# Performance work log

Hardware: AMD Instinct MI355X
Metric: run time of the kernel (lower is better)

The kernel has to match this reference:

```python
import jax, jax.numpy as jnp
import numpy as np

E = 8        # num_experts
C = 1024     # n_emb
H = 4096     # n_emb * ff_mult
B, T = 4, 1024


def setup_inputs() -> dict:
    key = jax.random.key(0)
    k_x, k_g, k_1, k_2, k_3 = jax.random.split(key, 5)
    scale = 0.02
    return {
        "x": jax.random.normal(k_x, (B, T, C), dtype=jnp.float32),
        "Wg": jax.random.normal(k_g, (E, C), dtype=jnp.float32) * scale,   # gate: Linear(C, E), weight [E, C]
        "W1": jax.random.normal(k_1, (E, C, H), dtype=jnp.float32) * scale,  # per-expert w1 (transposed for einsum)
        "W2": jax.random.normal(k_2, (E, H, C), dtype=jnp.float32) * scale,  # per-expert w2
        "W3": jax.random.normal(k_3, (E, C, H), dtype=jnp.float32) * scale,  # per-expert w3
        "top_k": 2,
    }


def reference(x, Wg, W1, W2, W3, top_k):
    Bd, Td, Cd = x.shape
    xf = x.reshape(-1, Cd)                                   # [N, C]
    N = xf.shape[0]
    logits = jnp.einsum('nc,ec->ne', xf, Wg)                 # router logits [N, E]
    probs = jax.nn.softmax(logits.astype(jnp.float32), axis=-1)
    w, sel = jax.lax.top_k(probs, top_k)                     # [N, k]
    w = w / w.sum(axis=-1, keepdims=True)                    # renormalize over selected
    # combine weight per (token, expert): sum of normalized topk weights routed to e
    cw = jnp.zeros((N, E), jnp.float32).at[jnp.arange(N)[:, None], sel].add(w)
    # dense grouped SwiGLU over all experts; combine weights zero out unselected experts
    h1 = jnp.einsum('nc,ech->neh', xf, W1)                   # [N, E, H]
    g = jax.nn.silu(h1) * jnp.einsum('nc,ech->neh', xf, W3)  # [N, E, H]
    out = jnp.einsum('neh,ehc,ne->nc', g, W2, cw.astype(x.dtype))
    return out.reshape(Bd, Td, Cd)
```

## Files before the change

### kernel.cpp

```cpp
#include <hip/hip_runtime.h>
#include <hip/hip_bf16.h>

#define E_     8
#define C_     1024
#define H_     4096
#define N_TOK  4096
#define TOPK   2
#define NSLOT  (N_TOK*TOPK)
#define SPAD   (NSLOT+128)

#define BM 128
#define BN 128
#define BK 32
#define LPAD 40

typedef __attribute__((ext_vector_type(4))) float f32x4;
typedef __attribute__((ext_vector_type(8))) short short8;

__device__ __forceinline__ unsigned short f2bf(float f) {
    return __builtin_bit_cast(unsigned short, __float2bfloat16(f));
}

__device__ __forceinline__ void gload16(const void* g, const void* l) {
    __builtin_amdgcn_global_load_lds(
        (const __attribute__((address_space(1))) unsigned int*)g,
        (__attribute__((address_space(3))) unsigned int*)l, 16, 0, 0);
}

__global__ void router_kernel(const float* __restrict__ x, const float* __restrict__ Wg,
                              int* __restrict__ sel, float* __restrict__ wts) {
    int wave = (blockIdx.x * blockDim.x + threadIdx.x) >> 6;
    int lane = threadIdx.x & 63;
    if (wave >= N_TOK) return;
    const float* xr = x + (size_t)wave * C_;
    float acc[E_];
#pragma unroll
    for (int e = 0; e < E_; ++e) acc[e] = 0.f;
    for (int c = lane; c < C_; c += 64) {
        float xv = xr[c];
#pragma unroll
        for (int e = 0; e < E_; ++e) acc[e] += xv * Wg[e * C_ + c];
    }
#pragma unroll
    for (int e = 0; e < E_; ++e) {
#pragma unroll
        for (int off = 32; off > 0; off >>= 1) acc[e] += __shfl_xor(acc[e], off);
    }
    if (lane == 0) {
        float mx = acc[0];
#pragma unroll
        for (int e = 1; e < E_; ++e) mx = fmaxf(mx, acc[e]);
        float p[E_]; float s = 0.f;
#pragma unroll
        for (int e = 0; e < E_; ++e) { p[e] = __expf(acc[e] - mx); s += p[e]; }
        float inv = 1.f / s;
#pragma unroll
        for (int e = 0; e < E_; ++e) p[e] *= inv;
        int b0 = 0; float v0 = p[0];
#pragma unroll
        for (int e = 1; e < E_; ++e) if (p[e] > v0) { v0 = p[e]; b0 = e; }
        int b1 = -1; float v1 = -1.f;
#pragma unroll
        for (int e = 0; e < E_; ++e) { if (e != b0 && p[e] > v1) { v1 = p[e]; b1 = e; } }
        float isum = 1.f / (v0 + v1);
        sel[wave*2]   = b0; sel[wave*2+1] = b1;
        wts[wave*2]   = v0 * isum; wts[wave*2+1] = v1 * isum;
    }
}

__global__ void assign_kernel(const int* __restrict__ sel, const float* __restrict__ wts,
                              int* __restrict__ counts, int* __restrict__ offsets,
                              int* __restrict__ pos_of_slot, int* __restrict__ token_of,
                              float* __restrict__ slotw) {
    __shared__ int cnt[256][E_];
    __shared__ int offs[E_];
    int t = threadIdx.x;
    const int PER = NSLOT / 256;
    int base = t * PER;
    int loc[E_];
#pragma unroll
    for (int e = 0; e < E_; ++e) loc[e] = 0;
    for (int i = 0; i < PER; ++i) loc[sel[base + i]]++;
#pragma unroll
    for (int e = 0; e < E_; ++e) cnt[t][e] = loc[e];
    __syncthreads();
    if (t < E_) {
        int run = 0;
        for (int i = 0; i < 256; ++i) { int c = cnt[i][t]; cnt[i][t] = run; run += c; }
        counts[t] = run;
    }
    __syncthreads();
    if (t == 0) {
        int s = 0;
        for (int e = 0; e < E_; ++e) { offs[e] = s; offsets[e] = s; s += counts[e]; }
    }
    __syncthreads();
    int run[E_];
#pragma unroll
    for (int e = 0; e < E_; ++e) run[e] = offs[e] + cnt[t][e];
    for (int i = 0; i < PER; ++i) {
        int s = base + i;
        int e = sel[s];
        int p = run[e]++;
        pos_of_slot[s] = p;
        token_of[p] = s >> 1;
        slotw[p] = wts[s];
    }
}

__global__ void copy_kernel(const float* __restrict__ x, const int* __restrict__ pos_of_slot,
                            unsigned short* __restrict__ Xg) {
    int slot = blockIdx.x * 4 + (threadIdx.x >> 6);
    int lane = threadIdx.x & 63;
    int pos = pos_of_slot[slot];
    int n = slot >> 1;
    const float* xr = x + (size_t)n * C_;
    unsigned short* dst = Xg + (size_t)pos * C_;
#pragma unroll
    for (int i = 0; i < 4; ++i) {
        int c0 = i * 256 + lane * 4;
        float4 v = *(const float4*)(xr + c0);
        ushort4 b;
        b.x = f2bf(v.x); b.y = f2bf(v.y); b.z = f2bf(v.z); b.w = f2bf(v.w);
        *(ushort4*)(dst + c0) = b;
    }
}

__global__ void wconv_kernel(const float* __restrict__ src, unsigned short* __restrict__ dst,
                             int R, int Cc) {
    int e = blockIdx.z;
    int c0 = blockIdx.x * 64;
    int r0 = blockIdx.y * 64;
    const float* s = src + (size_t)e * R * Cc;
    unsigned short* d = dst + (size_t)e * R * Cc;
    __shared__ unsigned short t_[64][72];
    int t = threadIdx.x;
    int tr = t >> 4, tc4 = (t & 15) * 4;
#pragma unroll
    for (int i = 0; i < 4; ++i) {
        int r = tr + i * 16;
        float4 v = *(const float4*)(s + (size_t)(r0 + r) * Cc + c0 + tc4);
        t_[r][tc4+0] = f2bf(v.x); t_[r][tc4+1] = f2bf(v.y);
        t_[r][tc4+2] = f2bf(v.z); t_[r][tc4+3] = f2bf(v.w);
    }
    __syncthreads();
    int oc = t >> 2, seg = (t & 3) * 16;
    short8 w0, w1;
#pragma unroll
    for (int j = 0; j < 8; ++j) {
        w0[j] = (short)t_[seg + j][oc];
        w1[j] = (short)t_[seg + 8 + j][oc];
    }
    unsigned short* dp = d + (size_t)(c0 + oc) * R + r0 + seg;
    *(short8*)dp = w0;
    *(short8*)(dp + 8) = w1;
}


__global__ __launch_bounds__(256, 2) void gemm1_fast(
        const unsigned short* __restrict__ Xg, const unsigned short* __restrict__ W1t,
        const unsigned short* __restrict__ W3t, unsigned short* __restrict__ G,
        const int* __restrict__ counts, const int* __restrict__ offsets) {
    int ct = blockIdx.x;
    int rslot = blockIdx.y;
    int e = rslot >> 5, rt = rslot & 31;
    int ne = counts[e];
    if (rt * BM >= ne) return;
    int row0 = offsets[e] + rt * BM;
    int n0 = ct * BN;

    __shared__ unsigned short As[BM * BK];
    __shared__ unsigned short B1s[BN * BK];
    __shared__ unsigned short B3s[BN * BK];

    int tid = threadIdx.x;
    int lane = tid & 63, wid = tid >> 6;
    int wr = (wid >> 1) * 64, wc = (wid & 1) * 64;

    f32x4 acc1[4][4], acc3[4][4];
#pragma unroll
    for (int m = 0; m < 4; ++m)
#pragma unroll
        for (int n = 0; n < 4; ++n) {
            acc1[m][n] = (f32x4){0.f,0.f,0.f,0.f};
            acc3[m][n] = (f32x4){0.f,0.f,0.f,0.f};
        }

    const unsigned short* B1p = W1t + ((size_t)e * H_ + n0) * C_;
    const unsigned short* B3p = W3t + ((size_t)e * H_ + n0) * C_;

    int q = lane >> 4, fr = lane & 15;

    for (int k0 = 0; k0 < C_; k0 += BK) {
#pragma unroll
        for (int h = 0; h < 2; ++h) {
            int cid = h * 4 + wid;
            int row = cid * 16 + (lane >> 2);
            int kc  = (lane & 3) ^ ((row >> 1) & 3);
            gload16(Xg + (size_t)(row0 + row) * C_ + k0 + kc * 8,
                    (const char*)As + cid * 1024);
            gload16(B1p + (size_t)row * C_ + k0 + kc * 8,
                    (const char*)B1s + cid * 1024);
            gload16(B3p + (size_t)row * C_ + k0 + kc * 8,
                    (const char*)B3s + cid * 1024);
        }
        __syncthreads();
        short8 a[4], b1[4], b3[4];
#pragma unroll
        for (int m = 0; m < 4; ++m) {
            int row = wr + m * 16 + fr;
            a[m] = *(const short8*)((const char*)As + row * 64 + ((q ^ ((row >> 1) & 3)) << 4));
        }
#pragma unroll
        for (int n = 0; n < 4; ++n) {
            int row = wc + n * 16 + fr;
            int sw = (q ^ ((row >> 1) & 3)) << 4;
            b1[n] = *(const short8*)((const char*)B1s + row * 64 + sw);
            b3[n] = *(const short8*)((const char*)B3s + row * 64 + sw);
        }
#pragma unroll
        for (int m = 0; m < 4; ++m)
#pragma unroll
            for (int n = 0; n < 4; ++n) {
                acc1[m][n] = __builtin_amdgcn_mfma_f32_16x16x32_bf16(a[m], b1[n], acc1[m][n], 0, 0, 0);
                acc3[m][n] = __builtin_amdgcn_mfma_f32_16x16x32_bf16(a[m], b3[n], acc3[m][n], 0, 0, 0);
            }
        __syncthreads();
    }
    int cfr = lane & 15;
#pragma unroll
    for (int m = 0; m < 4; ++m) {
#pragma unroll
        for (int rg = 0; rg < 4; ++rg) {
            int row = wr + m * 16 + q * 4 + rg;
            if (rt * BM + row < ne) {
                size_t gbase = (size_t)(row0 + row) * H_ + n0;
#pragma unroll
                for (int n = 0; n < 4; ++n) {
                    float h1 = acc1[m][n][rg];
                    float h3 = acc3[m][n][rg];
                    float g = h1 * h3 / (1.f + __expf(-h1));
                    G[gbase + wc + n * 16 + cfr] = f2bf(g);
                }
            }
        }
    }
}

__global__ __launch_bounds__(256, 2) void gemm2_fast(
        const unsigned short* __restrict__ G, const unsigned short* __restrict__ W2t,
        float* __restrict__ out, const int* __restrict__ counts,
        const int* __restrict__ offsets, const int* __restrict__ token_of,
        const float* __restrict__ slotw) {
    int ct = blockIdx.x;
    int rslot = blockIdx.y;
    int e = rslot >> 5, rt = rslot & 31;
    int ne = counts[e];
    if (rt * BM >= ne) return;
    int row0 = offsets[e] + rt * BM;
    int n0 = ct * BN;

    __shared__ unsigned short As[BM * BK];
    __shared__ unsigned short Bs[BN * BK];

    int tid = threadIdx.x;
    int lane = tid & 63, wid = tid >> 6;
    int wr = (wid >> 1) * 64, wc = (wid & 1) * 64;

    f32x4 acc[4][4];
#pragma unroll
    for (int m = 0; m < 4; ++m)
#pragma unroll
        for (int n = 0; n < 4; ++n) acc[m][n] = (f32x4){0.f,0.f,0.f,0.f};

    const unsigned short* Bp = W2t + ((size_t)e * C_ + n0) * H_;
    int q = lane >> 4, fr = lane & 15;

    for (int k0 = 0; k0 < H_; k0 += BK) {
#pragma unroll
        for (int h = 0; h < 2; ++h) {
            int cid = h * 4 + wid;
            int row = cid * 16 + (lane >> 2);
            int kc  = (lane & 3) ^ ((row >> 1) & 3);
            gload16(G + (size_t)(row0 + row) * H_ + k0 + kc * 8,
                    (const char*)As + cid * 1024);
            gload16(Bp + (size_t)row * H_ + k0 + kc * 8,
                    (const char*)Bs + cid * 1024);
        }
        __syncthreads();
        short8 a[4], b[4];
#pragma unroll
        for (int m = 0; m < 4; ++m) {
            int row = wr + m * 16 + fr;
            a[m] = *(const short8*)((const char*)As + row * 64 + ((q ^ ((row >> 1) & 3)) << 4));
        }
#pragma unroll
        for (int n = 0; n < 4; ++n) {
            int row = wc + n * 16 + fr;
            b[n] = *(const short8*)((const char*)Bs + row * 64 + ((q ^ ((row >> 1) & 3)) << 4));
        }
#pragma unroll
        for (int m = 0; m < 4; ++m)
#pragma unroll
            for (int n = 0; n < 4; ++n)
                acc[m][n] = __builtin_amdgcn_mfma_f32_16x16x32_bf16(a[m], b[n], acc[m][n], 0, 0, 0);
        __syncthreads();
    }
    int cfr = lane & 15;
#pragma unroll
    for (int m = 0; m < 4; ++m) {
#pragma unroll
        for (int rg = 0; rg < 4; ++rg) {
            int row = wr + m * 16 + q * 4 + rg;
            if (rt * BM + row < ne) {
                int grow = row0 + row;
                int tok = token_of[grow];
                float w = slotw[grow];
                float* orow = out + (size_t)tok * C_ + n0;
#pragma unroll
                for (int n = 0; n < 4; ++n)
                    atomicAdd(orow + wc + n * 16 + cfr, acc[m][n][rg] * w);
            }
        }
    }
}

__global__ __launch_bounds__(256, 2) void gemm1_slow(
        const unsigned short* __restrict__ Xg, const float* __restrict__ W1,
        const float* __restrict__ W3, unsigned short* __restrict__ G,
        const int* __restrict__ counts, const int* __restrict__ offsets) {
    int ct = blockIdx.x;
    int rslot = blockIdx.y;
    int e = rslot >> 5, rt = rslot & 31;
    int ne = counts[e];
    if (rt * BM >= ne) return;
    int row0 = offsets[e] + rt * BM;
    int n0 = ct * BN;

    __shared__ unsigned short As[BM][LPAD];
    __shared__ unsigned short B1s[BN][LPAD];
    __shared__ unsigned short B3s[BN][LPAD];

    int tid = threadIdx.x;
    int lane = tid & 63, wid = tid >> 6;
    int wr = (wid >> 1) * 64, wc = (wid & 1) * 64;

    f32x4 acc1[4][4], acc3[4][4];
#pragma unroll
    for (int m = 0; m < 4; ++m)
#pragma unroll
        for (int n = 0; n < 4; ++n) {
            acc1[m][n] = (f32x4){0.f,0.f,0.f,0.f};
            acc3[m][n] = (f32x4){0.f,0.f,0.f,0.f};
        }

    const float* B1p = W1 + (size_t)e * C_ * H_ + n0;
    const float* B3p = W3 + (size_t)e * C_ * H_ + n0;
    int chunk = tid & 3, rr = tid >> 2;
    int kq = tid >> 5, n4 = tid & 31;

    for (int k0 = 0; k0 < C_; k0 += BK) {
        __syncthreads();
#pragma unroll
        for (int h = 0; h < 2; ++h) {
            int row = rr + h * 64;
            uint4 v = *(const uint4*)(Xg + (size_t)(row0 + row) * C_ + k0 + chunk * 8);
            *(uint4*)&As[row][chunk * 8] = v;
        }
        {
            float4 r0 = *(const float4*)(B1p + (size_t)(k0 + kq*4 + 0) * H_ + n4*4);
            float4 r1 = *(const float4*)(B1p + (size_t)(k0 + kq*4 + 1) * H_ + n4*4);
            float4 r2 = *(const float4*)(B1p + (size_t)(k0 + kq*4 + 2) * H_ + n4*4);
            float4 r3 = *(const float4*)(B1p + (size_t)(k0 + kq*4 + 3) * H_ + n4*4);
            ushort4 w0 = {f2bf(r0.x), f2bf(r1.x), f2bf(r2.x), f2bf(r3.x)};
            ushort4 w1 = {f2bf(r0.y), f2bf(r1.y), f2bf(r2.y), f2bf(r3.y)};
            ushort4 w2 = {f2bf(r0.z), f2bf(r1.z), f2bf(r2.z), f2bf(r3.z)};
            ushort4 w3 = {f2bf(r0.w), f2bf(r1.w), f2bf(r2.w), f2bf(r3.w)};
            *(ushort4*)&B1s[n4*4+0][kq*4] = w0;
            *(ushort4*)&B1s[n4*4+1][kq*4] = w1;
            *(ushort4*)&B1s[n4*4+2][kq*4] = w2;
            *(ushort4*)&B1s[n4*4+3][kq*4] = w3;
            r0 = *(const float4*)(B3p + (size_t)(k0 + kq*4 + 0) * H_ + n4*4);
            r1 = *(const float4*)(B3p + (size_t)(k0 + kq*4 + 1) * H_ + n4*4);
            r2 = *(const float4*)(B3p + (size_t)(k0 + kq*4 + 2) * H_ + n4*4);
            r3 = *(const float4*)(B3p + (size_t)(k0 + kq*4 + 3) * H_ + n4*4);
            w0 = (ushort4){f2bf(r0.x), f2bf(r1.x), f2bf(r2.x), f2bf(r3.x)};
            w1 = (ushort4){f2bf(r0.y), f2bf(r1.y), f2bf(r2.y), f2bf(r3.y)};
            w2 = (ushort4){f2bf(r0.z), f2bf(r1.z), f2bf(r2.z), f2bf(r3.z)};
            w3 = (ushort4){f2bf(r0.w), f2bf(r1.w), f2bf(r2.w), f2bf(r3.w)};
            *(ushort4*)&B3s[n4*4+0][kq*4] = w0;
            *(ushort4*)&B3s[n4*4+1][kq*4] = w1;
            *(ushort4*)&B3s[n4*4+2][kq*4] = w2;
            *(ushort4*)&B3s[n4*4+3][kq*4] = w3;
        }
        __syncthreads();
        int q = lane >> 4, fr = lane & 15;
        short8 a[4], b1[4], b3[4];
#pragma unroll
        for (int m = 0; m < 4; ++m) a[m] = *(const short8*)&As[wr + m*16 + fr][q*8];
#pragma unroll
        for (int n = 0; n < 4; ++n) {
            b1[n] = *(const short8*)&B1s[wc + n*16 + fr][q*8];
            b3[n] = *(const short8*)&B3s[wc + n*16 + fr][q*8];
        }
#pragma unroll
        for (int m = 0; m < 4; ++m)
#pragma unroll
            for (int n = 0; n < 4; ++n) {
                acc1[m][n] = __builtin_amdgcn_mfma_f32_16x16x32_bf16(a[m], b1[n], acc1[m][n], 0, 0, 0);
                acc3[m][n] = __builtin_amdgcn_mfma_f32_16x16x32_bf16(a[m], b3[n], acc3[m][n], 0, 0, 0);
            }
    }
    int q = lane >> 4, cfr = lane & 15;
#pragma unroll
    for (int m = 0; m < 4; ++m) {
#pragma unroll
        for (int rg = 0; rg < 4; ++rg) {
            int row = wr + m*16 + q*4 + rg;
            if (rt * BM + row < ne) {
                size_t gbase = (size_t)(row0 + row) * H_ + n0;
#pragma unroll
                for (int n = 0; n < 4; ++n) {
                    float h1 = acc1[m][n][rg];
                    float h3 = acc3[m][n][rg];
                    float g = h1 * h3 / (1.f + __expf(-h1));
                    G[gbase + wc + n*16 + cfr] = f2bf(g);
                }
            }
        }
    }
}

__global__ __launch_bounds__(256, 2) void gemm2_slow(
        const unsigned short* __restrict__ G, const float* __restrict__ W2,
        float* __restrict__ out, const int* __restrict__ counts,
        const int* __restrict__ offsets, const int* __restrict__ token_of,
        const float* __restrict__ slotw) {
    int ct = blockIdx.x;
    int rslot = blockIdx.y;
    int e = rslot >> 5, rt = rslot & 31;
    int ne = counts[e];
    if (rt * BM >= ne) return;
    int row0 = offsets[e] + rt * BM;
    int n0 = ct * BN;

    __shared__ unsigned short As[BM][LPAD];
    __shared__ unsigned short Bs[BN][LPAD];

    int tid = threadIdx.x;
    int lane = tid & 63, wid = tid >> 6;
    int wr = (wid >> 1) * 64, wc = (wid & 1) * 64;

    f32x4 acc[4][4];
#pragma unroll
    for (int m = 0; m < 4; ++m)
#pragma unroll
        for (int n = 0; n < 4; ++n) acc[m][n] = (f32x4){0.f,0.f,0.f,0.f};

    const float* Bp = W2 + (size_t)e * H_ * C_ + n0;
    int chunk = tid & 3, rr = tid >> 2;
    int kq = tid >> 5, n4 = tid & 31;

    for (int k0 = 0; k0 < H_; k0 += BK) {
        __syncthreads();
#pragma unroll
        for (int h = 0; h < 2; ++h) {
            int row = rr + h * 64;
            uint4 v = *(const uint4*)(G + (size_t)(row0 + row) * H_ + k0 + chunk * 8);
            *(uint4*)&As[row][chunk * 8] = v;
        }
        {
            float4 r0 = *(const float4*)(Bp + (size_t)(k0 + kq*4 + 0) * C_ + n4*4);
            float4 r1 = *(const float4*)(Bp + (size_t)(k0 + kq*4 + 1) * C_ + n4*4);
            float4 r2 = *(const float4*)(Bp + (size_t)(k0 + kq*4 + 2) * C_ + n4*4);
            float4 r3 = *(const float4*)(Bp + (size_t)(k0 + kq*4 + 3) * C_ + n4*4);
            ushort4 w0 = {f2bf(r0.x), f2bf(r1.x), f2bf(r2.x), f2bf(r3.x)};
            ushort4 w1 = {f2bf(r0.y), f2bf(r1.y), f2bf(r2.y), f2bf(r3.y)};
            ushort4 w2 = {f2bf(r0.z), f2bf(r1.z), f2bf(r2.z), f2bf(r3.z)};
            ushort4 w3 = {f2bf(r0.w), f2bf(r1.w), f2bf(r2.w), f2bf(r3.w)};
            *(ushort4*)&Bs[n4*4+0][kq*4] = w0;
            *(ushort4*)&Bs[n4*4+1][kq*4] = w1;
            *(ushort4*)&Bs[n4*4+2][kq*4] = w2;
            *(ushort4*)&Bs[n4*4+3][kq*4] = w3;
        }
        __syncthreads();
        int q = lane >> 4, fr = lane & 15;
        short8 a[4], b[4];
#pragma unroll
        for (int m = 0; m < 4; ++m) a[m] = *(const short8*)&As[wr + m*16 + fr][q*8];
#pragma unroll
        for (int n = 0; n < 4; ++n) b[n] = *(const short8*)&Bs[wc + n*16 + fr][q*8];
#pragma unroll
        for (int m = 0; m < 4; ++m)
#pragma unroll
            for (int n = 0; n < 4; ++n)
                acc[m][n] = __builtin_amdgcn_mfma_f32_16x16x32_bf16(a[m], b[n], acc[m][n], 0, 0, 0);
    }
    int q = lane >> 4, cfr = lane & 15;
#pragma unroll
    for (int m = 0; m < 4; ++m) {
#pragma unroll
        for (int rg = 0; rg < 4; ++rg) {
            int row = wr + m*16 + q*4 + rg;
            if (rt * BM + row < ne) {
                int grow = row0 + row;
                int tok = token_of[grow];
                float w = slotw[grow];
                float* orow = out + (size_t)tok * C_ + n0;
#pragma unroll
                for (int n = 0; n < 4; ++n)
                    atomicAdd(orow + wc + n*16 + cfr, acc[m][n][rg] * w);
            }
        }
    }
}

extern "C" void kernel_launch(void* const* d_in, const int* in_sizes, int n_in,
                              void* d_out, int out_size, void* d_ws, size_t ws_size,
                              hipStream_t stream) {
    const float* x  = (const float*)d_in[0];
    const float* Wg = (const float*)d_in[1];
    const float* W1 = (const float*)d_in[2];
    const float* W2 = (const float*)d_in[3];
    const float* W3 = (const float*)d_in[4];
    float* out = (float*)d_out;

    char* ws = (char*)d_ws;
    size_t o = 0;
    int*   sel      = (int*)(ws + o);  o += (size_t)NSLOT * 4;
    float* wts      = (float*)(ws + o); o += (size_t)NSLOT * 4;
    int*   pos      = (int*)(ws + o);  o += (size_t)NSLOT * 4;
    int*   token_of = (int*)(ws + o);  o += (size_t)NSLOT * 4;
    float* slotw    = (float*)(ws + o); o += (size_t)NSLOT * 4;
    int*   counts   = (int*)(ws + o);
    int*   offsets  = counts + E_;     o += 256;
    unsigned short* Xg = (unsigned short*)(ws + o); o += (size_t)SPAD * C_ * 2;
    unsigned short* G  = (unsigned short*)(ws + o); o += (size_t)SPAD * H_ * 2;
    size_t need_slow = o;
    unsigned short* W1t = (unsigned short*)(ws + o); o += (size_t)E_ * H_ * C_ * 2;
    unsigned short* W3t = (unsigned short*)(ws + o); o += (size_t)E_ * H_ * C_ * 2;
    unsigned short* W2t = W1t;
    size_t need_fast = o;

    hipMemsetAsync(d_out, 0, (size_t)out_size * sizeof(float), stream);
    if (ws_size < need_slow) return;

    router_kernel<<<N_TOK/4, 256, 0, stream>>>(x, Wg, sel, wts);
    assign_kernel<<<1, 256, 0, stream>>>(sel, wts, counts, offsets, pos, token_of, slotw);
    copy_kernel<<<NSLOT/4, 256, 0, stream>>>(x, pos, Xg);

    if (ws_size >= need_fast) {
        wconv_kernel<<<dim3(H_/64, C_/64, E_), 256, 0, stream>>>(W1, W1t, C_, H_);
        wconv_kernel<<<dim3(H_/64, C_/64, E_), 256, 0, stream>>>(W3, W3t, C_, H_);
        gemm1_fast<<<dim3(H_/BN, E_*32), 256, 0, stream>>>(Xg, W1t, W3t, G, counts, offsets);
        wconv_kernel<<<dim3(C_/64, H_/64, E_), 256, 0, stream>>>(W2, W2t, H_, C_);
        gemm2_fast<<<dim3(C_/BN, E_*32), 256, 0, stream>>>(G, W2t, out, counts, offsets, token_of, slotw);
    } else {
        gemm1_slow<<<dim3(H_/BN, E_*32), 256, 0, stream>>>(Xg, W1, W3, G, counts, offsets);
        gemm2_slow<<<dim3(C_/BN, E_*32), 256, 0, stream>>>(G, W2, out, counts, offsets, token_of, slotw);
    }
}
```

Baseline: 537.9 us.

## Rewrite grouped GEMMs with 256x128 tiles, double-buffered LDS and phased prefetch

Both expert GEMM kernels are replaced by 8-wave versions that use 256-row by 128-column tiles with a K step of 64. Operand tiles are double-buffered in dynamic LDS and loaded through an XOR swizzle. Each K step is split into four phases that issue the next tile's global-to-LDS loads, wait with explicit vmcnt counts, then run MFMAs at raised wave priority. The aim is to hide memory latency behind compute and raise data reuse per tile. The cost is much larger LDS use (128KB and 96KB per block), which may limit occupancy. Because rt still goes 0..31 with 256-row tiles, many blocks exit early, which wastes some launch slots.

```diff
diff --git a/kernel.cpp b/kernel.cpp
--- a/kernel.cpp
+++ b/kernel.cpp
@@ -9,9 +9,6 @@
 #define NSLOT  (N_TOK*TOPK)
 #define SPAD   (NSLOT+128)
 
-#define BM 128
-#define BN 128
-#define BK 32
 #define LPAD 40
 
 typedef __attribute__((ext_vector_type(4))) float f32x4;
@@ -26,6 +23,9 @@
         (const __attribute__((address_space(1))) unsigned int*)g,
         (__attribute__((address_space(3))) unsigned int*)l, 16, 0, 0);
 }
+
+#define WAITVM_(n) asm volatile("s_waitcnt vmcnt(" #n ")" ::: "memory")
+#define WAITVM(n) WAITVM_(n)
 
 __global__ void router_kernel(const float* __restrict__ x, const float* __restrict__ Wg,
                               int* __restrict__ sel, float* __restrict__ wts) {
@@ -157,7 +157,67 @@
 }
 
 
-__global__ __launch_bounds__(256, 2) void gemm1_fast(
+#define G1_BM 256
+#define G1_BN 128
+#define G1_BK 64
+#define G1_NT (C_/G1_BK)
+
+#define G1_PHASE(F, ACCX, WN)                                                       \
+  {                                                                                 \
+    __builtin_amdgcn_s_barrier();                                                   \
+    {                                                                               \
+      int pn = (t + 1) & 1;                                                         \
+      int tsrc = (t + 1 < G1_NT) ? (t + 1) : t;                                     \
+      int k0n = tsrc * G1_BK;                                                       \
+      if ((F) == 0 || (F) == 1) {                                                   \
+        _Pragma("unroll")                                                           \
+        for (int r = 0; r < 2; ++r) {                                               \
+          int row = (F)*128 + r*64 + srow;                                          \
+          int lch = pch ^ (row & 7);                                                \
+          gload16(Ap + (size_t)row * C_ + k0n + lch*8,                              \
+                  (char*)As + pn*32768 + (((F)*128 + r*64 + wid*8) << 7));          \
+        }                                                                           \
+      } else {                                                                      \
+        const unsigned short* gsrc = ((F) == 2) ? B1p : B3p;                        \
+        char* ldst = (char*)(((F) == 2) ? B1s : B3s) + pn*16384;                    \
+        _Pragma("unroll")                                                           \
+        for (int r = 0; r < 2; ++r) {                                               \
+          int row = r*64 + srow;                                                    \
+          int lch = pch ^ (row & 7);                                                \
+          gload16(gsrc + (size_t)row * C_ + k0n + lch*8,                            \
+                  ldst + ((r*64 + wid*8) << 7));                                    \
+        }                                                                           \
+      }                                                                             \
+    }                                                                               \
+    WAITVM(WN);                                                                     \
+    __builtin_amdgcn_s_barrier();                                                   \
+    __builtin_amdgcn_sched_barrier(0);                                              \
+    {                                                                               \
+      int p = t & 1; int ks = (F) & 1;                                              \
+      const unsigned short* Ab = As + p*16384;                                      \
+      const unsigned short* Bb = (((F) < 2) ? B1s : B3s) + p*8192;                  \
+      short8 a[4], b[4];                                                            \
+      _Pragma("unroll")                                                             \
+      for (int m = 0; m < 4; ++m) {                                                 \
+        int row = wm*64 + m*16 + fr;                                                \
+        a[m] = *(const short8*)(Ab + row*64 + (((ks*4 + q) ^ (row & 7)) << 3));     \
+      }                                                                             \
+      _Pragma("unroll")                                                             \
+      for (int n = 0; n < 4; ++n) {                                                 \
+        int row = wn*64 + n*16 + fr;                                                \
+        b[n] = *(const short8*)(Bb + row*64 + (((ks*4 + q) ^ (row & 7)) << 3));     \
+      }                                                                             \
+      __builtin_amdgcn_s_setprio(1);                                                \
+      _Pragma("unroll")                                                             \
+      for (int m = 0; m < 4; ++m)                                                   \
+        _Pragma("unroll")                                                           \
+        for (int n = 0; n < 4; ++n)                                                 \
+          ACCX[m][n] = __builtin_amdgcn_mfma_f32_16x16x32_bf16(a[m], b[n], ACCX[m][n], 0, 0, 0); \
+      __builtin_amdgcn_s_setprio(0);                                                \
+    }                                                                               \
+  }
+
+__global__ __launch_bounds__(512, 2) void gemm1_f8(
         const unsigned short* __restrict__ Xg, const unsigned short* __restrict__ W1t,
         const unsigned short* __restrict__ W3t, unsigned short* __restrict__ G,
         const int* __restrict__ counts, const int* __restrict__ offsets) {
@@ -165,17 +225,24 @@
     int rslot = blockIdx.y;
     int e = rslot >> 5, rt = rslot & 31;
     int ne = counts[e];
-    if (rt * BM >= ne) return;
-    int row0 = offsets[e] + rt * BM;
-    int n0 = ct * BN;
-
-    __shared__ unsigned short As[BM * BK];
-    __shared__ unsigned short B1s[BN * BK];
-    __shared__ unsigned short B3s[BN * BK];
-
-    int tid = threadIdx.x;
-    int lane = tid & 63, wid = tid >> 6;
-    int wr = (wid >> 1) * 64, wc = (wid & 1) * 64;
+    if (rt * G1_BM >= ne) return;
+    int row0 = offsets[e] + rt * G1_BM;
+    int n0 = ct * G1_BN;
+
+    extern __shared__ unsigned short lds[];
+    unsigned short* As  = lds;
+    unsigned short* B1s = lds + 2*256*64;
+    unsigned short* B3s = B1s + 2*128*64;
+
+    int tid = threadIdx.x, lane = tid & 63, wid = tid >> 6;
+    int wm = wid >> 1, wn = wid & 1;
+    int fr = lane & 15, q = lane >> 4;
+    int srow = wid * 8 + (lane >> 3);
+    int pch  = lane & 7;
+
+    const unsigned short* Ap  = Xg + (size_t)row0 * C_;
+    const unsigned short* B1p = W1t + ((size_t)e * H_ + n0) * C_;
+    const unsigned short* B3p = W3t + ((size_t)e * H_ + n0) * C_;
 
     f32x4 acc1[4][4], acc3[4][4];
 #pragma unroll
@@ -186,68 +253,114 @@
             acc3[m][n] = (f32x4){0.f,0.f,0.f,0.f};
         }
 
-    const unsigned short* B1p = W1t + ((size_t)e * H_ + n0) * C_;
-    const unsigned short* B3p = W3t + ((size_t)e * H_ + n0) * C_;
-
-    int q = lane >> 4, fr = lane & 15;
-
-    for (int k0 = 0; k0 < C_; k0 += BK) {
-#pragma unroll
-        for (int h = 0; h < 2; ++h) {
-            int cid = h * 4 + wid;
-            int row = cid * 16 + (lane >> 2);
-            int kc  = (lane & 3) ^ ((row >> 1) & 3);
-            gload16(Xg + (size_t)(row0 + row) * C_ + k0 + kc * 8,
-                    (const char*)As + cid * 1024);
-            gload16(B1p + (size_t)row * C_ + k0 + kc * 8,
-                    (const char*)B1s + cid * 1024);
-            gload16(B3p + (size_t)row * C_ + k0 + kc * 8,
-                    (const char*)B3s + cid * 1024);
-        }
-        __syncthreads();
-        short8 a[4], b1[4], b3[4];
-#pragma unroll
-        for (int m = 0; m < 4; ++m) {
-            int row = wr + m * 16 + fr;
-            a[m] = *(const short8*)((const char*)As + row * 64 + ((q ^ ((row >> 1) & 3)) << 4));
-        }
-#pragma unroll
-        for (int n = 0; n < 4; ++n) {
-            int row = wc + n * 16 + fr;
-            int sw = (q ^ ((row >> 1) & 3)) << 4;
-            b1[n] = *(const short8*)((const char*)B1s + row * 64 + sw);
-            b3[n] = *(const short8*)((const char*)B3s + row * 64 + sw);
-        }
-#pragma unroll
-        for (int m = 0; m < 4; ++m)
-#pragma unroll
-            for (int n = 0; n < 4; ++n) {
-                acc1[m][n] = __builtin_amdgcn_mfma_f32_16x16x32_bf16(a[m], b1[n], acc1[m][n], 0, 0, 0);
-                acc3[m][n] = __builtin_amdgcn_mfma_f32_16x16x32_bf16(a[m], b3[n], acc3[m][n], 0, 0, 0);
-            }
-        __syncthreads();
-    }
+#pragma unroll
+    for (int u = 0; u < 2; ++u)
+#pragma unroll
+        for (int r = 0; r < 2; ++r) {
+            int row = u*128 + r*64 + srow;
+            int lch = pch ^ (row & 7);
+            gload16(Ap + (size_t)row * C_ + lch*8,
+                    (char*)As + ((u*128 + r*64 + wid*8) << 7));
+        }
+#pragma unroll
+    for (int r = 0; r < 2; ++r) {
+        int row = r*64 + srow;
+        int lch = pch ^ (row & 7);
+        gload16(B1p + (size_t)row * C_ + lch*8, (char*)B1s + ((r*64 + wid*8) << 7));
+    }
+#pragma unroll
+    for (int r = 0; r < 2; ++r) {
+        int row = r*64 + srow;
+        int lch = pch ^ (row & 7);
+        gload16(B3p + (size_t)row * C_ + lch*8, (char*)B3s + ((r*64 + wid*8) << 7));
+    }
+
+    for (int t = 0; t < G1_NT; ++t) {
+        G1_PHASE(0, acc1, 4)
+        G1_PHASE(1, acc1, 6)
+        G1_PHASE(2, acc3, 6)
+        G1_PHASE(3, acc3, 8)
+    }
+    WAITVM(0);
+
     int cfr = lane & 15;
 #pragma unroll
-    for (int m = 0; m < 4; ++m) {
+    for (int m = 0; m < 4; ++m)
 #pragma unroll
         for (int rg = 0; rg < 4; ++rg) {
-            int row = wr + m * 16 + q * 4 + rg;
-            if (rt * BM + row < ne) {
-                size_t gbase = (size_t)(row0 + row) * H_ + n0;
+            int row = wm*64 + m*16 + q*4 + rg;
+            if (rt * G1_BM + row < ne) {
+                size_t gbase = (size_t)(row0 + row) * H_ + n0 + wn*64;
 #pragma unroll
                 for (int n = 0; n < 4; ++n) {
                     float h1 = acc1[m][n][rg];
                     float h3 = acc3[m][n][rg];
                     float g = h1 * h3 / (1.f + __expf(-h1));
-                    G[gbase + wc + n * 16 + cfr] = f2bf(g);
+                    G[gbase + n*16 + cfr] = f2bf(g);
                 }
             }
         }
-    }
-}
-
-__global__ __launch_bounds__(256, 2) void gemm2_fast(
+}
+
+#define G2_BM 256
+#define G2_BN 128
+#define G2_BK 64
+#define G2_NT (H_/G2_BK)
+
+#define G2_PHASE(F, WN)                                                             \
+  {                                                                                 \
+    __builtin_amdgcn_s_barrier();                                                   \
+    if ((F) < 3) {                                                                  \
+      int pn = (t + 1) & 1;                                                         \
+      int tsrc = (t + 1 < G2_NT) ? (t + 1) : t;                                     \
+      int k0n = tsrc * G2_BK;                                                       \
+      if ((F) == 0 || (F) == 1) {                                                   \
+        _Pragma("unroll")                                                           \
+        for (int r = 0; r < 2; ++r) {                                               \
+          int row = (F)*128 + r*64 + srow;                                          \
+          int lch = pch ^ (row & 7);                                                \
+          gload16(Ap + (size_t)row * H_ + k0n + lch*8,                              \
+                  (char*)As + pn*32768 + (((F)*128 + r*64 + wid*8) << 7));          \
+        }                                                                           \
+      } else {                                                                      \
+        _Pragma("unroll")                                                           \
+        for (int r = 0; r < 2; ++r) {                                               \
+          int row = r*64 + srow;                                                    \
+          int lch = pch ^ (row & 7);                                                \
+          gload16(Bp + (size_t)row * H_ + k0n + lch*8,                              \
+                  (char*)Bs + pn*16384 + ((r*64 + wid*8) << 7));                    \
+        }                                                                           \
+      }                                                                             \
+    }                                                                               \
+    WAITVM(WN);                                                                     \
+    __builtin_amdgcn_s_barrier();                                                   \
+    __builtin_amdgcn_sched_barrier(0);                                              \
+    {                                                                               \
+      int p = t & 1; int ks = (F) >> 1; int nh = (F) & 1;                           \
+      const unsigned short* Ab = As + p*16384;                                      \
+      const unsigned short* Bb = Bs + p*8192;                                       \
+      short8 a[4], b[2];                                                            \
+      _Pragma("unroll")                                                             \
+      for (int m = 0; m < 4; ++m) {                                                 \
+        int row = wm*64 + m*16 + fr;                                                \
+        a[m] = *(const short8*)(Ab + row*64 + (((ks*4 + q) ^ (row & 7)) << 3));     \
+      }                                                                             \
+      _Pragma("unroll")                                                             \
+      for (int j = 0; j < 2; ++j) {                                                 \
+        int row = wn*64 + (nh*2 + j)*16 + fr;                                       \
+        b[j] = *(const short8*)(Bb + row*64 + (((ks*4 + q) ^ (row & 7)) << 3));     \
+      }                                                                             \
+      __builtin_amdgcn_s_setprio(1);                                                \
+      _Pragma("unroll")                                                             \
+      for (int m = 0; m < 4; ++m)                                                   \
+        _Pragma("unroll")                                                           \
+        for (int j = 0; j < 2; ++j)                                                 \
+          acc[m][nh*2 + j] = __builtin_amdgcn_mfma_f32_16x16x32_bf16(a[m], b[j], acc[m][nh*2 + j], 0, 0, 0); \
+      __builtin_amdgcn_s_setprio(0);                                                \
+    }                                                                               \
+  }
+
+__global__ __launch_bounds__(512, 2) void gemm2_f8(
         const unsigned short* __restrict__ G, const unsigned short* __restrict__ W2t,
         float* __restrict__ out, const int* __restrict__ counts,
         const int* __restrict__ offsets, const int* __restrict__ token_of,
@@ -256,16 +369,22 @@
     int rslot = blockIdx.y;
     int e = rslot >> 5, rt = rslot & 31;
     int ne = counts[e];
-    if (rt * BM >= ne) return;
-    int row0 = offsets[e] + rt * BM;
-    int n0 = ct * BN;
-
-    __shared__ unsigned short As[BM * BK];
-    __shared__ unsigned short Bs[BN * BK];
-
-    int tid = threadIdx.x;
-    int lane = tid & 63, wid = tid >> 6;
-    int wr = (wid >> 1) * 64, wc = (wid & 1) * 64;
+    if (rt * G2_BM >= ne) return;
+    int row0 = offsets[e] + rt * G2_BM;
+    int n0 = ct * G2_BN;
+
+    extern __shared__ unsigned short lds[];
+    unsigned short* As = lds;
+    unsigned short* Bs = lds + 2*256*64;
+
+    int tid = threadIdx.x, lane = tid & 63, wid = tid >> 6;
+    int wm = wid >> 1, wn = wid & 1;
+    int fr = lane & 15, q = lane >> 4;
+    int srow = wid * 8 + (lane >> 3);
+    int pch  = lane & 7;
+
+    const unsigned short* Ap = G + (size_t)row0 * H_;
+    const unsigned short* Bp = W2t + ((size_t)e * C_ + n0) * H_;
 
     f32x4 acc[4][4];
 #pragma unroll
@@ -273,58 +392,51 @@
 #pragma unroll
         for (int n = 0; n < 4; ++n) acc[m][n] = (f32x4){0.f,0.f,0.f,0.f};
 
-    const unsigned short* Bp = W2t + ((size_t)e * C_ + n0) * H_;
-    int q = lane >> 4, fr = lane & 15;
-
-    for (int k0 = 0; k0 < H_; k0 += BK) {
-#pragma unroll
-        for (int h = 0; h < 2; ++h) {
-            int cid = h * 4 + wid;
-            int row = cid * 16 + (lane >> 2);
-            int kc  = (lane & 3) ^ ((row >> 1) & 3);
-            gload16(G + (size_t)(row0 + row) * H_ + k0 + kc * 8,
-                    (const char*)As + cid * 1024);
-            gload16(Bp + (size_t)row * H_ + k0 + kc * 8,
-                    (const char*)Bs + cid * 1024);
-        }
-        __syncthreads();
-        short8 a[4], b[4];
-#pragma unroll
-        for (int m = 0; m < 4; ++m) {
-            int row = wr + m * 16 + fr;
-            a[m] = *(const short8*)((const char*)As + row * 64 + ((q ^ ((row >> 1) & 3)) << 4));
-        }
-#pragma unroll
-        for (int n = 0; n < 4; ++n) {
-            int row = wc + n * 16 + fr;
-            b[n] = *(const short8*)((const char*)Bs + row * 64 + ((q ^ ((row >> 1) & 3)) << 4));
-        }
-#pragma unroll
-        for (int m = 0; m < 4; ++m)
-#pragma unroll
-            for (int n = 0; n < 4; ++n)
-                acc[m][n] = __builtin_amdgcn_mfma_f32_16x16x32_bf16(a[m], b[n], acc[m][n], 0, 0, 0);
-        __syncthreads();
-    }
+#pragma unroll
+    for (int u = 0; u < 2; ++u)
+#pragma unroll
+        for (int r = 0; r < 2; ++r) {
+            int row = u*128 + r*64 + srow;
+            int lch = pch ^ (row & 7);
+            gload16(Ap + (size_t)row * H_ + lch*8,
+                    (char*)As + ((u*128 + r*64 + wid*8) << 7));
+        }
+#pragma unroll
+    for (int r = 0; r < 2; ++r) {
+        int row = r*64 + srow;
+        int lch = pch ^ (row & 7);
+        gload16(Bp + (size_t)row * H_ + lch*8, (char*)Bs + ((r*64 + wid*8) << 7));
+    }
+
+    for (int t = 0; t < G2_NT; ++t) {
+        G2_PHASE(0, 2)
+        G2_PHASE(1, 4)
+        G2_PHASE(2, 6)
+        G2_PHASE(3, 6)
+    }
+    WAITVM(0);
+
     int cfr = lane & 15;
 #pragma unroll
-    for (int m = 0; m < 4; ++m) {
+    for (int m = 0; m < 4; ++m)
 #pragma unroll
         for (int rg = 0; rg < 4; ++rg) {
-            int row = wr + m * 16 + q * 4 + rg;
-            if (rt * BM + row < ne) {
+            int row = wm*64 + m*16 + q*4 + rg;
+            if (rt * G2_BM + row < ne) {
                 int grow = row0 + row;
                 int tok = token_of[grow];
                 float w = slotw[grow];
-                float* orow = out + (size_t)tok * C_ + n0;
+                float* orow = out + (size_t)tok * C_ + n0 + wn*64;
 #pragma unroll
                 for (int n = 0; n < 4; ++n)
-                    atomicAdd(orow + wc + n * 16 + cfr, acc[m][n][rg] * w);
+                    atomicAdd(orow + n*16 + cfr, acc[m][n][rg] * w);
             }
         }
-    }
-}
-
+}
+
+#define BM 128
+#define BN 128
+#define BK 32
 __global__ __launch_bounds__(256, 2) void gemm1_slow(
         const unsigned short* __restrict__ Xg, const float* __restrict__ W1,
         const float* __restrict__ W3, unsigned short* __restrict__ G,
@@ -550,11 +662,13 @@
     copy_kernel<<<NSLOT/4, 256, 0, stream>>>(x, pos, Xg);
 
     if (ws_size >= need_fast) {
+        hipFuncSetAttribute((const void*)gemm1_f8, hipFuncAttributeMaxDynamicSharedMemorySize, 131072);
+        hipFuncSetAttribute((const void*)gemm2_f8, hipFuncAttributeMaxDynamicSharedMemorySize, 98304);
         wconv_kernel<<<dim3(H_/64, C_/64, E_), 256, 0, stream>>>(W1, W1t, C_, H_);
         wconv_kernel<<<dim3(H_/64, C_/64, E_), 256, 0, stream>>>(W3, W3t, C_, H_);
-        gemm1_fast<<<dim3(H_/BN, E_*32), 256, 0, stream>>>(Xg, W1t, W3t, G, counts, offsets);
+        gemm1_f8<<<dim3(H_/G1_BN, E_*32), 512, 131072, stream>>>(Xg, W1t, W3t, G, counts, offsets);
         wconv_kernel<<<dim3(C_/64, H_/64, E_), 256, 0, stream>>>(W2, W2t, H_, C_);
-        gemm2_fast<<<dim3(C_/BN, E_*32), 256, 0, stream>>>(G, W2t, out, counts, offsets, token_of, slotw);
+        gemm2_f8<<<dim3(C_/G2_BN, E_*32), 512, 98304, stream>>>(G, W2t, out, counts, offsets, token_of, slotw);
     } else {
         gemm1_slow<<<dim3(H_/BN, E_*32), 256, 0, stream>>>(Xg, W1, W3, G, counts, offsets);
         gemm2_slow<<<dim3(C_/BN, E_*32), 256, 0, stream>>>(G, W2, out, counts, offsets, token_of, slotw);
```

Measured after the change: 487.5 us. 9.4% less time.

## Replace grouped GEMMs with 4-slot LDS ring-buffered pipelined kernels using 256-row tiles

Applied to the files above, without the earlier changes.

Both expert GEMMs now keep a 4-slot ring buffer in dynamic LDS, prefetching three K-steps ahead with direct global-to-LDS loads and waiting with partial vmcnt counts instead of a full sync each step. Blocks grow to 512 threads with 256-row M tiles, MFMA sections get raised priority, and the LDS swizzle changes. The goal is to hide global-load latency and raise data reuse per block, at the cost of large LDS use (128KB and 96KB) that limits occupancy, plus more padding waste for experts whose row counts are not multiples of 256.

```diff
diff --git a/kernel.cpp b/kernel.cpp
--- a/kernel.cpp
+++ b/kernel.cpp
@@ -7,11 +7,8 @@
 #define N_TOK  4096
 #define TOPK   2
 #define NSLOT  (N_TOK*TOPK)
-#define SPAD   (NSLOT+128)
-
-#define BM 128
-#define BN 128
-#define BK 32
+#define SPAD   (NSLOT+256)
+
 #define LPAD 40
 
 typedef __attribute__((ext_vector_type(4))) float f32x4;
@@ -26,6 +23,10 @@
         (const __attribute__((address_space(1))) unsigned int*)g,
         (__attribute__((address_space(3))) unsigned int*)l, 16, 0, 0);
 }
+
+#define WAITVM_(n) asm volatile("s_waitcnt vmcnt(" #n ")" ::: "memory")
+#define WAITVM(n) WAITVM_(n)
+#define SWZ(r) ((((r)&3) ^ (((r)>>2)&3)))
 
 __global__ void router_kernel(const float* __restrict__ x, const float* __restrict__ Wg,
                               int* __restrict__ sel, float* __restrict__ wts) {
@@ -157,7 +158,9 @@
 }
 
 
-__global__ __launch_bounds__(256, 2) void gemm1_fast(
+#define G1_NH (C_/32)
+
+__global__ __launch_bounds__(512, 2) void gemm1_ring(
         const unsigned short* __restrict__ Xg, const unsigned short* __restrict__ W1t,
         const unsigned short* __restrict__ W3t, unsigned short* __restrict__ G,
         const int* __restrict__ counts, const int* __restrict__ offsets) {
@@ -165,17 +168,23 @@
     int rslot = blockIdx.y;
     int e = rslot >> 5, rt = rslot & 31;
     int ne = counts[e];
-    if (rt * BM >= ne) return;
-    int row0 = offsets[e] + rt * BM;
-    int n0 = ct * BN;
-
-    __shared__ unsigned short As[BM * BK];
-    __shared__ unsigned short B1s[BN * BK];
-    __shared__ unsigned short B3s[BN * BK];
-
-    int tid = threadIdx.x;
-    int lane = tid & 63, wid = tid >> 6;
-    int wr = (wid >> 1) * 64, wc = (wid & 1) * 64;
+    if (rt * 256 >= ne) return;
+    int row0 = offsets[e] + rt * 256;
+    int n0 = ct * 128;
+
+    extern __shared__ char lds[];
+    char* As  = lds;
+    char* B1s = lds + 65536;
+    char* B3s = lds + 98304;
+
+    int tid = threadIdx.x, lane = tid & 63, wid = tid >> 6;
+    int wm = wid >> 1, wn = wid & 1;
+    int fr = lane & 15, q = lane >> 4;
+    int srow = lane >> 2, pchk = lane & 3;
+
+    const unsigned short* Ap  = Xg + (size_t)row0 * C_;
+    const unsigned short* B1p = W1t + ((size_t)e * H_ + n0) * C_;
+    const unsigned short* B3p = W3t + ((size_t)e * H_ + n0) * C_;
 
     f32x4 acc1[4][4], acc3[4][4];
 #pragma unroll
@@ -186,38 +195,47 @@
             acc3[m][n] = (f32x4){0.f,0.f,0.f,0.f};
         }
 
-    const unsigned short* B1p = W1t + ((size_t)e * H_ + n0) * C_;
-    const unsigned short* B3p = W3t + ((size_t)e * H_ + n0) * C_;
-
-    int q = lane >> 4, fr = lane & 15;
-
-    for (int k0 = 0; k0 < C_; k0 += BK) {
-#pragma unroll
-        for (int h = 0; h < 2; ++h) {
-            int cid = h * 4 + wid;
-            int row = cid * 16 + (lane >> 2);
-            int kc  = (lane & 3) ^ ((row >> 1) & 3);
-            gload16(Xg + (size_t)(row0 + row) * C_ + k0 + kc * 8,
-                    (const char*)As + cid * 1024);
-            gload16(B1p + (size_t)row * C_ + k0 + kc * 8,
-                    (const char*)B1s + cid * 1024);
-            gload16(B3p + (size_t)row * C_ + k0 + kc * 8,
-                    (const char*)B3s + cid * 1024);
-        }
-        __syncthreads();
+    auto STAGE = [&](int hs, int slot) {
+        int k0 = hs * 32;
+#pragma unroll
+        for (int r = 0; r < 2; ++r) {
+            int row = r*128 + wid*16 + srow;
+            int sc = pchk ^ SWZ(row);
+            gload16(Ap + (size_t)row * C_ + k0 + sc*8,
+                    As + slot*16384 + (r*128 + wid*16)*64);
+        }
+        {
+            int row = wid*16 + srow;
+            int sc = pchk ^ SWZ(row);
+            gload16(B1p + (size_t)row * C_ + k0 + sc*8, B1s + slot*8192 + wid*1024);
+            gload16(B3p + (size_t)row * C_ + k0 + sc*8, B3s + slot*8192 + wid*1024);
+        }
+    };
+
+    STAGE(0, 0); STAGE(1, 1); STAGE(2, 2);
+    WAITVM(8);
+    __builtin_amdgcn_s_barrier();
+
+    for (int h = 0; h < G1_NH; ++h) {
+        int slot = h & 3;
         short8 a[4], b1[4], b3[4];
 #pragma unroll
         for (int m = 0; m < 4; ++m) {
-            int row = wr + m * 16 + fr;
-            a[m] = *(const short8*)((const char*)As + row * 64 + ((q ^ ((row >> 1) & 3)) << 4));
+            int row = wm*64 + m*16 + fr;
+            a[m] = *(const short8*)(As + slot*16384 + row*64 + ((q ^ SWZ(row)) << 4));
         }
 #pragma unroll
         for (int n = 0; n < 4; ++n) {
-            int row = wc + n * 16 + fr;
-            int sw = (q ^ ((row >> 1) & 3)) << 4;
-            b1[n] = *(const short8*)((const char*)B1s + row * 64 + sw);
-            b3[n] = *(const short8*)((const char*)B3s + row * 64 + sw);
-        }
+            int row = wn*64 + n*16 + fr;
+            int so = row*64 + ((q ^ SWZ(row)) << 4);
+            b1[n] = *(const short8*)(B1s + slot*8192 + so);
+            b3[n] = *(const short8*)(B3s + slot*8192 + so);
+        }
+        int hs = (h + 3 < G1_NH) ? h + 3 : G1_NH - 1;
+        STAGE(hs, (h + 3) & 3);
+        WAITVM(8);
+        __builtin_amdgcn_sched_barrier(0);
+        __builtin_amdgcn_s_setprio(1);
 #pragma unroll
         for (int m = 0; m < 4; ++m)
 #pragma unroll
@@ -225,29 +243,32 @@
                 acc1[m][n] = __builtin_amdgcn_mfma_f32_16x16x32_bf16(a[m], b1[n], acc1[m][n], 0, 0, 0);
                 acc3[m][n] = __builtin_amdgcn_mfma_f32_16x16x32_bf16(a[m], b3[n], acc3[m][n], 0, 0, 0);
             }
-        __syncthreads();
-    }
-    int cfr = lane & 15;
-#pragma unroll
-    for (int m = 0; m < 4; ++m) {
+        __builtin_amdgcn_s_setprio(0);
+        __builtin_amdgcn_s_barrier();
+    }
+    WAITVM(0);
+
+#pragma unroll
+    for (int m = 0; m < 4; ++m)
 #pragma unroll
         for (int rg = 0; rg < 4; ++rg) {
-            int row = wr + m * 16 + q * 4 + rg;
-            if (rt * BM + row < ne) {
-                size_t gbase = (size_t)(row0 + row) * H_ + n0;
+            int row = wm*64 + m*16 + q*4 + rg;
+            if (rt * 256 + row < ne) {
+                size_t gbase = (size_t)(row0 + row) * H_ + n0 + wn*64;
 #pragma unroll
                 for (int n = 0; n < 4; ++n) {
                     float h1 = acc1[m][n][rg];
                     float h3 = acc3[m][n][rg];
                     float g = h1 * h3 / (1.f + __expf(-h1));
-                    G[gbase + wc + n * 16 + cfr] = f2bf(g);
+                    G[gbase + n*16 + fr] = f2bf(g);
                 }
             }
         }
-    }
-}
-
-__global__ __launch_bounds__(256, 2) void gemm2_fast(
+}
+
+#define G2_NH (H_/32)
+
+__global__ __launch_bounds__(512, 2) void gemm2_ring(
         const unsigned short* __restrict__ G, const unsigned short* __restrict__ W2t,
         float* __restrict__ out, const int* __restrict__ counts,
         const int* __restrict__ offsets, const int* __restrict__ token_of,
@@ -256,16 +277,21 @@
     int rslot = blockIdx.y;
     int e = rslot >> 5, rt = rslot & 31;
     int ne = counts[e];
-    if (rt * BM >= ne) return;
-    int row0 = offsets[e] + rt * BM;
-    int n0 = ct * BN;
-
-    __shared__ unsigned short As[BM * BK];
-    __shared__ unsigned short Bs[BN * BK];
-
-    int tid = threadIdx.x;
-    int lane = tid & 63, wid = tid >> 6;
-    int wr = (wid >> 1) * 64, wc = (wid & 1) * 64;
+    if (rt * 256 >= ne) return;
+    int row0 = offsets[e] + rt * 256;
+    int n0 = ct * 128;
+
+    extern __shared__ char lds[];
+    char* As = lds;
+    char* Bs = lds + 65536;
+
+    int tid = threadIdx.x, lane = tid & 63, wid = tid >> 6;
+    int wm = wid >> 1, wn = wid & 1;
+    int fr = lane & 15, q = lane >> 4;
+    int srow = lane >> 2, pchk = lane & 3;
+
+    const unsigned short* Ap = G + (size_t)row0 * H_;
+    const unsigned short* Bp = W2t + ((size_t)e * C_ + n0) * H_;
 
     f32x4 acc[4][4];
 #pragma unroll
@@ -273,58 +299,74 @@
 #pragma unroll
         for (int n = 0; n < 4; ++n) acc[m][n] = (f32x4){0.f,0.f,0.f,0.f};
 
-    const unsigned short* Bp = W2t + ((size_t)e * C_ + n0) * H_;
-    int q = lane >> 4, fr = lane & 15;
-
-    for (int k0 = 0; k0 < H_; k0 += BK) {
-#pragma unroll
-        for (int h = 0; h < 2; ++h) {
-            int cid = h * 4 + wid;
-            int row = cid * 16 + (lane >> 2);
-            int kc  = (lane & 3) ^ ((row >> 1) & 3);
-            gload16(G + (size_t)(row0 + row) * H_ + k0 + kc * 8,
-                    (const char*)As + cid * 1024);
-            gload16(Bp + (size_t)row * H_ + k0 + kc * 8,
-                    (const char*)Bs + cid * 1024);
-        }
-        __syncthreads();
+    auto STAGE = [&](int hs, int slot) {
+        int k0 = hs * 32;
+#pragma unroll
+        for (int r = 0; r < 2; ++r) {
+            int row = r*128 + wid*16 + srow;
+            int sc = pchk ^ SWZ(row);
+            gload16(Ap + (size_t)row * H_ + k0 + sc*8,
+                    As + slot*16384 + (r*128 + wid*16)*64);
+        }
+        {
+            int row = wid*16 + srow;
+            int sc = pchk ^ SWZ(row);
+            gload16(Bp + (size_t)row * H_ + k0 + sc*8, Bs + slot*8192 + wid*1024);
+        }
+    };
+
+    STAGE(0, 0); STAGE(1, 1); STAGE(2, 2);
+    WAITVM(6);
+    __builtin_amdgcn_s_barrier();
+
+    for (int h = 0; h < G2_NH; ++h) {
+        int slot = h & 3;
         short8 a[4], b[4];
 #pragma unroll
         for (int m = 0; m < 4; ++m) {
-            int row = wr + m * 16 + fr;
-            a[m] = *(const short8*)((const char*)As + row * 64 + ((q ^ ((row >> 1) & 3)) << 4));
+            int row = wm*64 + m*16 + fr;
+            a[m] = *(const short8*)(As + slot*16384 + row*64 + ((q ^ SWZ(row)) << 4));
         }
 #pragma unroll
         for (int n = 0; n < 4; ++n) {
-            int row = wc + n * 16 + fr;
-            b[n] = *(const short8*)((const char*)Bs + row * 64 + ((q ^ ((row >> 1) & 3)) << 4));
-        }
+            int row = wn*64 + n*16 + fr;
+            b[n] = *(const short8*)(Bs + slot*8192 + row*64 + ((q ^ SWZ(row)) << 4));
+        }
+        int hs = (h + 3 < G2_NH) ? h + 3 : G2_NH - 1;
+        STAGE(hs, (h + 3) & 3);
+        WAITVM(6);
+        __builtin_amdgcn_sched_barrier(0);
+        __builtin_amdgcn_s_setprio(1);
 #pragma unroll
         for (int m = 0; m < 4; ++m)
 #pragma unroll
             for (int n = 0; n < 4; ++n)
                 acc[m][n] = __builtin_amdgcn_mfma_f32_16x16x32_bf16(a[m], b[n], acc[m][n], 0, 0, 0);
-        __syncthreads();
-    }
-    int cfr = lane & 15;
-#pragma unroll
-    for (int m = 0; m < 4; ++m) {
+        __builtin_amdgcn_s_setprio(0);
+        __builtin_amdgcn_s_barrier();
+    }
+    WAITVM(0);
+
+#pragma unroll
+    for (int m = 0; m < 4; ++m)
 #pragma unroll
         for (int rg = 0; rg < 4; ++rg) {
-            int row = wr + m * 16 + q * 4 + rg;
-            if (rt * BM + row < ne) {
+            int row = wm*64 + m*16 + q*4 + rg;
+            if (rt * 256 + row < ne) {
                 int grow = row0 + row;
                 int tok = token_of[grow];
                 float w = slotw[grow];
-                float* orow = out + (size_t)tok * C_ + n0;
+                float* orow = out + (size_t)tok * C_ + n0 + wn*64;
 #pragma unroll
                 for (int n = 0; n < 4; ++n)
-                    atomicAdd(orow + wc + n * 16 + cfr, acc[m][n][rg] * w);
+                    atomicAdd(orow + n*16 + fr, acc[m][n][rg] * w);
             }
         }
-    }
-}
-
+}
+
+#define BM 128
+#define BN 128
+#define BK 32
 __global__ __launch_bounds__(256, 2) void gemm1_slow(
         const unsigned short* __restrict__ Xg, const float* __restrict__ W1,
         const float* __restrict__ W3, unsigned short* __restrict__ G,
@@ -550,11 +592,13 @@
     copy_kernel<<<NSLOT/4, 256, 0, stream>>>(x, pos, Xg);
 
     if (ws_size >= need_fast) {
+        hipFuncSetAttribute((const void*)gemm1_ring, hipFuncAttributeMaxDynamicSharedMemorySize, 131072);
+        hipFuncSetAttribute((const void*)gemm2_ring, hipFuncAttributeMaxDynamicSharedMemorySize, 98304);
         wconv_kernel<<<dim3(H_/64, C_/64, E_), 256, 0, stream>>>(W1, W1t, C_, H_);
         wconv_kernel<<<dim3(H_/64, C_/64, E_), 256, 0, stream>>>(W3, W3t, C_, H_);
-        gemm1_fast<<<dim3(H_/BN, E_*32), 256, 0, stream>>>(Xg, W1t, W3t, G, counts, offsets);
+        gemm1_ring<<<dim3(H_/128, E_*32), 512, 131072, stream>>>(Xg, W1t, W3t, G, counts, offsets);
         wconv_kernel<<<dim3(C_/64, H_/64, E_), 256, 0, stream>>>(W2, W2t, H_, C_);
-        gemm2_fast<<<dim3(C_/BN, E_*32), 256, 0, stream>>>(G, W2t, out, counts, offsets, token_of, slotw);
+        gemm2_ring<<<dim3(C_/128, E_*32), 512, 98304, stream>>>(G, W2t, out, counts, offsets, token_of, slotw);
     } else {
         gemm1_slow<<<dim3(H_/BN, E_*32), 256, 0, stream>>>(Xg, W1, W3, G, counts, offsets);
         gemm2_slow<<<dim3(C_/BN, E_*32), 256, 0, stream>>>(G, W2, out, counts, offsets, token_of, slotw);
```

New measurement: 501.2 us. 6.8% less time.
